# Kernel optimization log

Measured on AMD Instinct MI355X. Metric: run time of the kernel, lower is better.

## Reference

```python
import jax, jax.numpy as jnp
import numpy as np

B, K, T, V, R = 32, 3, 20, 10000, 36
E_DIM, VDIM, H1, H2, PH = 512, 2048, 1024, 1024, 256
START, EOS = 1, 2
NEG = -1e9


def lstm_cell(x, h, c, Wi, Wh, b):
    # torch LSTM gate order: i, f, g, o
    g = x @ Wi.T + h @ Wh.T + b
    i, f, gg, o = jnp.split(g, 4, axis=-1)
    c = jax.nn.sigmoid(f) * c + jax.nn.sigmoid(i) * jnp.tanh(gg)
    h = jax.nn.sigmoid(o) * jnp.tanh(c)
    return h, c


def _decode(features, E, Wi1, Wh1, b1, Wi2, Wh2, b2, Wva, bva, Wha, bha, wa, Wout, bout):
    featP = features @ Wva.T + bva                       # [B,R,PH] (step-invariant)
    vmean = jnp.broadcast_to(features.mean(1)[:, None, :], (B, K, VDIM))
    eos_row = jnp.full((V,), NEG, features.dtype).at[EOS].set(0.0)

    def step(carry, t):
        tokens, logp_traj, h1, c1, h2, c2, finished, trajs = carry
        emb = E[tokens]                                   # [B,K,E]
        x1 = jnp.concatenate([h2, vmean, emb], -1)        # [B,K,H2+VDIM+E]
        h1, c1 = lstm_cell(x1, h1, c1, Wi1, Wh1, b1)
        # additive attention over R regions
        hp = h1 @ Wha.T + bha                             # [B,K,PH]
        pre = jnp.tanh(featP[:, None] + hp[:, :, None])   # [B,K,R,PH]
        alpha = jax.nn.softmax(jnp.einsum('bkrp,p->bkr', pre, wa), -1)
        vhat = jnp.einsum('bkr,brd->bkd', alpha, features)
        x2 = jnp.concatenate([h1, vhat], -1)
        h2, c2 = lstm_cell(x2, h2, c2, Wi2, Wh2, b2)
        logp = jax.nn.log_softmax(h2 @ Wout.T + bout, -1)  # [B,K,V]
        # max_k_NoDuplicate: forbid repeating the previous token (only for t>0)
        dup = jax.nn.one_hot(tokens, V, dtype=logp.dtype) * jnp.where(t > 0, 1.0, 0.0)
        logp = logp - 1e4 * dup
        # EOS-terminated beams: only EOS with logprob 0, everything else -inf
        logp = jnp.where(finished[:, :, None], eos_row, logp)
        scores = logp_traj[:, :, None] + logp              # [B,K,V]
        # at t==0 all beams are identical -> keep only beam 0 as source
        beam_mask = ((jnp.arange(K) > 0)[None, :, None]) & (t == 0)
        scores = jnp.where(beam_mask, NEG, scores)
        vals, idx = jax.lax.top_k(scores.reshape(B, K * V), K)
        parent = idx // V
        tok = idx % V
        gather = lambda x: jnp.take_along_axis(x, parent[:, :, None], axis=1)
        h1, c1, h2, c2 = gather(h1), gather(c1), gather(h2), gather(c2)
        finished = jnp.take_along_axis(finished, parent, 1) | (tok == EOS)
        trajs = jnp.take_along_axis(trajs, parent[:, :, None], 1)
        trajs = jnp.where(jnp.arange(T)[None, None, :] == t, tok[:, :, None], trajs)
        return (tok, vals, h1, c1, h2, c2, finished, trajs), None

    z1 = jnp.zeros((B, K, H1), features.dtype)
    z2 = jnp.zeros((B, K, H2), features.dtype)
    init = (jnp.full((B, K), START, jnp.int32), jnp.zeros((B, K), features.dtype),
            z1, z1, z2, z2, jnp.zeros((B, K), bool), jnp.zeros((B, K, T), jnp.int32))
    carry, _ = jax.lax.scan(step, init, jnp.arange(T))
    _, logp_traj, _, _, _, _, _, trajs = carry
    return trajs.transpose(0, 2, 1), logp_traj  # [B,T,K] like torch.stack(Trajs,2), [B,K]


def setup_inputs():
    key = jax.random.key(0)
    ks = jax.random.split(key, 12)
    s = 0.05
    rn = lambda k, shp: jax.random.normal(k, shp, jnp.float32) * s
    return {
        'features': jax.random.normal(ks[0], (B, R, VDIM), jnp.float32),
        'E': rn(ks[1], (V, E_DIM)),
        'Wi1': rn(ks[2], (4 * H1, H2 + VDIM + E_DIM)),
        'Wh1': rn(ks[3], (4 * H1, H1)),
        'b1': jnp.zeros((4 * H1,), jnp.float32),
        'Wi2': rn(ks[4], (4 * H2, H1 + VDIM)),
        'Wh2': rn(ks[5], (4 * H2, H2)),
        'b2': jnp.zeros((4 * H2,), jnp.float32),
        'Wva': rn(ks[6], (PH, VDIM)),
        'bva': jnp.zeros((PH,), jnp.float32),
        'Wha': rn(ks[7], (PH, H1)),
        'bha': jnp.zeros((PH,), jnp.float32),
        'wa': rn(ks[8], (PH,)),
        'Wout': rn(ks[9], (V, H2)),
        'bout': jnp.zeros((V,), jnp.float32),
    }


def reference(features, E, Wi1, Wh1, b1, Wi2, Wh2, b2, Wva, bva, Wha, bha, wa, Wout, bout):
    return _decode(features, E, Wi1, Wh1, b1, Wi2, Wh2, b2, Wva, bva, Wha, bha, wa, Wout, bout)
```

## Files before the change

### kernel.cpp

```cpp
#include <hip/hip_runtime.h>
#include <math.h>

#define BB 32
#define KB 3
#define TT 20
#define VV 10000
#define RR 36
#define ED 512
#define VD 2048
#define HH 1024
#define PH_ 256
#define ROWS 96
#define EOS_TOK 2

struct Seg { const double* X; const float* W; int ldx; int ldw; int woff; int kbeg; };
struct GemmA { Seg seg[3]; int nseg; int Mtot; int N; int Ktot; };

#define GBN 64
#define GKC 32
#define PX 34
#define PW 36

__global__ __launch_bounds__(256) void gemm_f64(GemmA a, double* __restrict__ part) {
  __shared__ double Xs[96][PX];
  __shared__ float  Ws[GBN][PW];
  const int tid = threadIdx.x;
  const int n0 = blockIdx.x * GBN;
  const int s = blockIdx.y;
  const int m0 = blockIdx.z * 96;
  const int S = gridDim.y;
  const int ck = a.Ktot / S;
  const int ks = s * ck;
  const int nch = ck / GKC;
  const int tx = tid & 15, ty = tid >> 4;

  double acc[6][4];
#pragma unroll
  for (int r = 0; r < 6; ++r)
#pragma unroll
    for (int c = 0; c < 4; ++c) acc[r][c] = 0.0;

  double2 xst[6];
  float4 wst[2];

  auto issue = [&](int k0) {
    int si = 0;
    for (int i = 1; i < a.nseg; ++i) if (k0 >= a.seg[i].kbeg) si = i;
    Seg sg = a.seg[si];
    int kl = k0 - sg.kbeg;
#pragma unroll
    for (int j = 0; j < 6; ++j) {
      int i = tid + 256 * j;
      int m = i >> 4, q = (i & 15) << 1;
      int mg = m0 + m;
      double2 v; v.x = 0.0; v.y = 0.0;
      if (mg < a.Mtot) v = *(const double2*)&sg.X[(size_t)mg * sg.ldx + kl + q];
      xst[j] = v;
    }
#pragma unroll
    for (int j = 0; j < 2; ++j) {
      int i = tid + 256 * j;
      int n = i >> 3, q = (i & 7) << 2;
      int ng = n0 + n;
      float4 v = {0.f, 0.f, 0.f, 0.f};
      if (ng < a.N) v = *(const float4*)&sg.W[(size_t)ng * sg.ldw + sg.woff + kl + q];
      wst[j] = v;
    }
  };

  issue(ks);
  for (int ch = 0; ch < nch; ++ch) {
    __syncthreads();
#pragma unroll
    for (int j = 0; j < 6; ++j) {
      int i = tid + 256 * j;
      int m = i >> 4, q = (i & 15) << 1;
      *(double2*)&Xs[m][q] = xst[j];
    }
#pragma unroll
    for (int j = 0; j < 2; ++j) {
      int i = tid + 256 * j;
      int n = i >> 3, q = (i & 7) << 2;
      *(float4*)&Ws[n][q] = wst[j];
    }
    __syncthreads();
    if (ch + 1 < nch) issue(ks + (ch + 1) * GKC);
#pragma unroll
    for (int kq = 0; kq < GKC; kq += 4) {
      double wd[4][4];
#pragma unroll
      for (int c = 0; c < 4; ++c) {
        float4 w = *(const float4*)&Ws[tx + 16 * c][kq];
        wd[c][0] = (double)w.x; wd[c][1] = (double)w.y;
        wd[c][2] = (double)w.z; wd[c][3] = (double)w.w;
      }
#pragma unroll
      for (int r = 0; r < 6; ++r) {
        double2 x01 = *(const double2*)&Xs[ty * 6 + r][kq];
        double2 x23 = *(const double2*)&Xs[ty * 6 + r][kq + 2];
#pragma unroll
        for (int c = 0; c < 4; ++c) {
          acc[r][c] = fma(x01.x, wd[c][0], acc[r][c]);
          acc[r][c] = fma(x01.y, wd[c][1], acc[r][c]);
          acc[r][c] = fma(x23.x, wd[c][2], acc[r][c]);
          acc[r][c] = fma(x23.y, wd[c][3], acc[r][c]);
        }
      }
    }
  }
#pragma unroll
  for (int r = 0; r < 6; ++r) {
    int mg = m0 + ty * 6 + r;
    if (mg >= a.Mtot) continue;
    size_t base = ((size_t)s * a.Mtot + mg) * a.N;
#pragma unroll
    for (int c = 0; c < 4; ++c) {
      int ng = n0 + tx + 16 * c;
      if (ng < a.N) part[base + ng] = acc[r][c];
    }
  }
}

__global__ void convf_kernel(const float* __restrict__ s, double* __restrict__ d, int n) {
  int i = blockIdx.x * 256 + threadIdx.x;
  if (i < n) d[i] = (double)s[i];
}

__global__ void conv_kernel(const float* b1, const float* b2, const float* bva,
                            const float* bha, const float* wa, const float* bout,
                            double* b1d, double* b2d, double* bvad,
                            double* bhad, double* wad, double* boutd) {
  int i = blockIdx.x * 256 + threadIdx.x;
  if (i < 4 * HH) { b1d[i] = (double)b1[i]; b2d[i] = (double)b2[i]; }
  if (i < PH_) { bvad[i] = (double)bva[i]; bhad[i] = (double)bha[i]; wad[i] = (double)wa[i]; }
  if (i < VV) boutd[i] = (double)bout[i];
}

__global__ void init_kernel(double* h1s, double* c1s, double* h2s, double* c2s,
                            int* tok, double* lpt, int* fin, int* trj) {
  int idx = blockIdx.x * 256 + threadIdx.x;
  if (idx < ROWS * HH) { h1s[idx] = 0.0; c1s[idx] = 0.0; h2s[idx] = 0.0; c2s[idx] = 0.0; }
  if (idx < ROWS) { tok[idx] = 1; lpt[idx] = 0.0; fin[idx] = 0; }
  if (idx < ROWS * TT) trj[idx] = 0;
}

__global__ void vmean_kernel(const float* __restrict__ features, double* __restrict__ vme) {
  int idx = blockIdx.x * 256 + threadIdx.x;
  if (idx >= BB * VD) return;
  int b = idx / VD, d = idx - b * VD;
  double sum = 0.0;
  for (int r = 0; r < RR; ++r) sum += (double)features[((size_t)b * RR + r) * VD + d];
  vme[idx] = sum / (double)RR;
}

__global__ void reduce_bias_kernel(double* __restrict__ out, const double* __restrict__ parts,
                                   const double* __restrict__ bias, int rows, int cols, int S) {
  int idx = blockIdx.x * 256 + threadIdx.x;
  if (idx >= rows * cols) return;
  int c = idx % cols;
  double acc = bias[c];
  for (int s = 0; s < S; ++s) acc += parts[(size_t)s * rows * cols + idx];
  out[idx] = acc;
}

__global__ void embed_kernel(const int* __restrict__ tok, const float* __restrict__ E,
                             double* __restrict__ emb) {
  int idx = blockIdx.x * 256 + threadIdx.x;
  if (idx >= ROWS * ED) return;
  int row = idx >> 9, e2 = idx & (ED - 1);
  emb[idx] = (double)E[(size_t)tok[row] * ED + e2];
}

__global__ void lstm_kernel(const double* __restrict__ gP, int S,
                            const double* __restrict__ bias_col, const double* __restrict__ bias_row,
                            const double* __restrict__ c_in, double* __restrict__ h_out,
                            double* __restrict__ c_out) {
  int idx = blockIdx.x * 256 + threadIdx.x;
  if (idx >= ROWS * (HH / 2)) return;
  int row = idx >> 9, jj = (idx & 511) << 1;
  int b = row / KB;
  double2 g[4];
#pragma unroll
  for (int gi = 0; gi < 4; ++gi) {
    double2 acc;
    if (bias_col) acc = *(const double2*)&bias_col[gi * HH + jj];
    else          acc = *(const double2*)&bias_row[(size_t)b * 4 * HH + gi * HH + jj];
    for (int s = 0; s < S; ++s) {
      double2 p = *(const double2*)&gP[((size_t)s * ROWS + row) * (4 * HH) + gi * HH + jj];
      acc.x += p.x; acc.y += p.y;
    }
    g[gi] = acc;
  }
  double2 cp = *(const double2*)&c_in[((size_t)row << 10) + jj];
  double2 hv, cv;
  {
    double ig = 1.0 / (1.0 + exp(-g[0].x)), fg = 1.0 / (1.0 + exp(-g[1].x));
    double gg = tanh(g[2].x), og = 1.0 / (1.0 + exp(-g[3].x));
    cv.x = fg * cp.x + ig * gg; hv.x = og * tanh(cv.x);
  }
  {
    double ig = 1.0 / (1.0 + exp(-g[0].y)), fg = 1.0 / (1.0 + exp(-g[1].y));
    double gg = tanh(g[2].y), og = 1.0 / (1.0 + exp(-g[3].y));
    cv.y = fg * cp.y + ig * gg; hv.y = og * tanh(cv.y);
  }
  *(double2*)&h_out[((size_t)row << 10) + jj] = hv;
  *(double2*)&c_out[((size_t)row << 10) + jj] = cv;
}

__global__ __launch_bounds__(256) void attn_kernel(const double* __restrict__ hpP, int S,
    const double* __restrict__ bha, const double* __restrict__ featP,
    const float* __restrict__ features, const double* __restrict__ wa,
    double* __restrict__ vhat) {
  int row = blockIdx.x;
  int b = row / KB;
  int tid = threadIdx.x;
  __shared__ double hp[PH_];
  __shared__ double e[RR];
  {
    double v = bha[tid];
    for (int s = 0; s < S; ++s) v += hpP[((size_t)s * ROWS + row) * PH_ + tid];
    hp[tid] = v;
  }
  __syncthreads();
  int wv = tid >> 6, ln = tid & 63;
  for (int r = wv * 9; r < wv * 9 + 9; ++r) {
    double p = 0.0;
#pragma unroll
    for (int i = 0; i < 4; ++i) {
      int ph = ln * 4 + i;
      p += tanh(featP[((size_t)b * RR + r) * PH_ + ph] + hp[ph]) * wa[ph];
    }
#pragma unroll
    for (int o = 32; o; o >>= 1) p += __shfl_down(p, o);
    if (ln == 0) e[r] = p;
  }
  __syncthreads();
  if (tid == 0) {
    double m = e[0];
    for (int r = 1; r < RR; ++r) m = fmax(m, e[r]);
    double se = 0.0;
    for (int r = 0; r < RR; ++r) se += exp(e[r] - m);
    for (int r = 0; r < RR; ++r) e[r] = exp(e[r] - m) / se;
  }
  __syncthreads();
  for (int d = tid; d < VD; d += 256) {
    double acc2 = 0.0;
    for (int r = 0; r < RR; ++r) acc2 += e[r] * (double)features[((size_t)b * RR + r) * VD + d];
    vhat[(size_t)row * VD + d] = acc2;
  }
}

__device__ inline double wred_maxd(double v) {
#pragma unroll
  for (int o = 32; o; o >>= 1) v = fmax(v, __shfl_down(v, o));
  return v;
}
__device__ inline double wred_sumd(double v) {
#pragma unroll
  for (int o = 32; o; o >>= 1) v += __shfl_down(v, o);
  return v;
}

__device__ inline bool better(double va, int ia, double vb, int ib) {
  if (va != vb) return va > vb;
  return (unsigned)ia < (unsigned)ib;
}

__global__ __launch_bounds__(256) void lchunk_kernel(const double* __restrict__ lP, int S,
    const double* __restrict__ bout, const int* __restrict__ tok_old, int t,
    double* __restrict__ cm, double* __restrict__ cs,
    double* __restrict__ cv, int* __restrict__ ci) {
  const int CHV = VV / 8;
  int row = blockIdx.x, chk = blockIdx.y, tid = threadIdx.x;
  int v0 = chk * CHV;
  int tokp = tok_old[row];
  double r[5];
  double lmax = -1.0e300;
#pragma unroll
  for (int j = 0; j < 5; ++j) {
    int vv = tid + (j << 8);
    double acc = -1.0e300;
    if (vv < CHV) {
      int v = v0 + vv;
      acc = bout[v];
      for (int s = 0; s < S; ++s) acc += lP[((size_t)s * ROWS + row) * VV + v];
      lmax = fmax(lmax, acc);
    }
    r[j] = acc;
  }
  __shared__ double red[4];
  double m = wred_maxd(lmax);
  if ((tid & 63) == 0) red[tid >> 6] = m;
  __syncthreads();
  m = fmax(fmax(red[0], red[1]), fmax(red[2], red[3]));
  double se = 0.0;
#pragma unroll
  for (int j = 0; j < 5; ++j) {
    int vv = tid + (j << 8);
    if (vv < CHV) se += exp(r[j] - m);
  }
  se = wred_sumd(se);
  __syncthreads();
  if ((tid & 63) == 0) red[tid >> 6] = se;
  __syncthreads();
  se = red[0] + red[1] + red[2] + red[3];
  double lv[3] = {-INFINITY, -INFINITY, -INFINITY};
  int li[3] = {-1, -1, -1};
#pragma unroll
  for (int j = 0; j < 5; ++j) {
    int vv = tid + (j << 8);
    if (vv >= CHV) continue;
    int v = v0 + vv;
    double sc = r[j];
    if (t > 0 && v == tokp) sc -= 1e4;
    if (better(sc, v, lv[2], li[2])) {
      if (better(sc, v, lv[1], li[1])) {
        lv[2] = lv[1]; li[2] = li[1];
        if (better(sc, v, lv[0], li[0])) { lv[1] = lv[0]; li[1] = li[0]; lv[0] = sc; li[0] = v; }
        else { lv[1] = sc; li[1] = v; }
      } else { lv[2] = sc; li[2] = v; }
    }
  }
  __shared__ double sv[256 * 3];
  __shared__ int si[256 * 3];
  sv[tid * 3 + 0] = lv[0]; sv[tid * 3 + 1] = lv[1]; sv[tid * 3 + 2] = lv[2];
  si[tid * 3 + 0] = li[0]; si[tid * 3 + 1] = li[1]; si[tid * 3 + 2] = li[2];
  for (int off2 = 128; off2 >= 1; off2 >>= 1) {
    __syncthreads();
    if (tid < off2) {
      double av[3], bv2[3]; int ai3[3], bi3[3];
#pragma unroll
      for (int j = 0; j < 3; ++j) {
        av[j] = sv[tid * 3 + j]; ai3[j] = si[tid * 3 + j];
        bv2[j] = sv[(tid + off2) * 3 + j]; bi3[j] = si[(tid + off2) * 3 + j];
      }
      double mv[3]; int mi[3];
      int ai = 0, bi = 0;
#pragma unroll
      for (int o = 0; o < 3; ++o) {
        if (better(av[ai], ai3[ai], bv2[bi], bi3[bi])) { mv[o] = av[ai]; mi[o] = ai3[ai]; ++ai; }
        else { mv[o] = bv2[bi]; mi[o] = bi3[bi]; ++bi; }
      }
#pragma unroll
      for (int j = 0; j < 3; ++j) { sv[tid * 3 + j] = mv[j]; si[tid * 3 + j] = mi[j]; }
    }
  }
  __syncthreads();
  if (tid == 0) {
    int o = row * 8 + chk;
    cm[o] = m; cs[o] = se;
    cv[o * 3 + 0] = sv[0]; cv[o * 3 + 1] = sv[1]; cv[o * 3 + 2] = sv[2];
    ci[o * 3 + 0] = si[0]; ci[o * 3 + 1] = si[1]; ci[o * 3 + 2] = si[2];
  }
}

__global__ __launch_bounds__(64) void topk2_kernel(
    const double* __restrict__ cm, const double* __restrict__ cs,
    const double* __restrict__ cv, const int* __restrict__ ci,
    const double* __restrict__ lpt_old, const int* __restrict__ fin_old,
    const int* __restrict__ trj_old, int t,
    int* __restrict__ tok_new, double* __restrict__ lpt_new, int* __restrict__ fin_new,
    int* __restrict__ trj_new, int* __restrict__ parent) {
  int b = blockIdx.x, tid = threadIdx.x;
  __shared__ double candv[72];
  __shared__ int candi[72];
  __shared__ int cnt[3];
  __shared__ int fink[3];
  __shared__ int sp[3], stk[3];
  if (tid < KB) {
    int row = b * KB + tid;
    double lpt = lpt_old[row];
    int fin = fin_old[row];
    fink[tid] = fin;
    int base = tid * 24;
    if (t == 0 && tid > 0) {
      cnt[tid] = 0;
    } else if (fin) {
      candv[base] = lpt;
      candi[base] = tid * VV + EOS_TOK;
      cnt[tid] = 1;
    } else {
      double M = -1.0e300;
      for (int c = 0; c < 8; ++c) M = fmax(M, cm[row * 8 + c]);
      double SE = 0.0;
      for (int c = 0; c < 8; ++c) SE += cs[row * 8 + c] * exp(cm[row * 8 + c] - M);
      double l = log(SE);
      int n = 0;
      for (int c = 0; c < 8; ++c) {
#pragma unroll
        for (int s3 = 0; s3 < 3; ++s3) {
          double val = cv[(row * 8 + c) * 3 + s3];
          int idx = ci[(row * 8 + c) * 3 + s3];
          candv[base + n] = lpt + ((val - M) - l);
          candi[base + n] = tid * VV + idx;
          ++n;
        }
      }
      cnt[tid] = n;
    }
  }
  __syncthreads();
  if (tid == 0) {
    double bv[3] = {-INFINITY, -INFINITY, -INFINITY};
    int bi2[3] = {-1, -1, -1};
    for (int k = 0; k < KB; ++k) {
      for (int j = 0; j < cnt[k]; ++j) {
        double sc = candv[k * 24 + j];
        int idx = candi[k * 24 + j];
        if (better(sc, idx, bv[2], bi2[2])) {
          if (better(sc, idx, bv[1], bi2[1])) {
            bv[2] = bv[1]; bi2[2] = bi2[1];
            if (better(sc, idx, bv[0], bi2[0])) { bv[1] = bv[0]; bi2[1] = bi2[0]; bv[0] = sc; bi2[0] = idx; }
            else { bv[1] = sc; bi2[1] = idx; }
          } else { bv[2] = sc; bi2[2] = idx; }
        }
      }
    }
#pragma unroll
    for (int o = 0; o < 3; ++o) {
      int idx = bi2[o];
      int p = idx / VV, tk = idx - p * VV;
      sp[o] = p; stk[o] = tk;
      parent[b * KB + o] = p;
      tok_new[b * KB + o] = tk;
      lpt_new[b * KB + o] = bv[o];
      fin_new[b * KB + o] = fink[p] | (tk == EOS_TOK);
    }
  }
  __syncthreads();
  if (tid < KB * TT) {
    int kk = tid / TT, tt = tid - kk * TT;
    trj_new[(b * KB + kk) * TT + tt] = (tt == t) ? stk[kk] : trj_old[(b * KB + sp[kk]) * TT + tt];
  }
}

__global__ void gather_kernel(const int* __restrict__ parent,
    const double* __restrict__ h1p, const double* __restrict__ c1p,
    const double* __restrict__ h2p, const double* __restrict__ c2p,
    double* __restrict__ h1s, double* __restrict__ c1s,
    double* __restrict__ h2s, double* __restrict__ c2s) {
  int idx = blockIdx.x * 256 + threadIdx.x;
  if (idx >= ROWS * (HH / 2)) return;
  int row = idx >> 9, jj = (idx & 511) << 1;
  int b = row / KB;
  int p = parent[row];
  size_t src = ((size_t)(b * KB + p) << 10) + jj;
  size_t dst = ((size_t)row << 10) + jj;
  *(double2*)&h1s[dst] = *(const double2*)&h1p[src];
  *(double2*)&c1s[dst] = *(const double2*)&c1p[src];
  *(double2*)&h2s[dst] = *(const double2*)&h2p[src];
  *(double2*)&c2s[dst] = *(const double2*)&c2p[src];
}

__global__ void out_kernel(const int* __restrict__ trj, const double* __restrict__ lpt,
                           float* __restrict__ out) {
  int idx = blockIdx.x * 256 + threadIdx.x;
  if (idx < BB * TT * KB) {
    int k = idx % KB;
    int rest = idx / KB;
    int t = rest % TT;
    int b = rest / TT;
    out[idx] = (float)trj[((size_t)(b * KB + k)) * TT + t];
  }
  if (idx < ROWS) out[BB * TT * KB + idx] = (float)lpt[idx];
}

extern "C" void kernel_launch(void* const* d_in, const int* in_sizes, int n_in,
                              void* d_out, int out_size, void* d_ws, size_t ws_size,
                              hipStream_t stream) {
  const float* features = (const float*)d_in[0];
  const float* E = (const float*)d_in[1];
  const float* Wi1 = (const float*)d_in[2];
  const float* Wh1 = (const float*)d_in[3];
  const float* b1 = (const float*)d_in[4];
  const float* Wi2 = (const float*)d_in[5];
  const float* Wh2 = (const float*)d_in[6];
  const float* b2 = (const float*)d_in[7];
  const float* Wva = (const float*)d_in[8];
  const float* bva = (const float*)d_in[9];
  const float* Wha = (const float*)d_in[10];
  const float* bha = (const float*)d_in[11];
  const float* wa = (const float*)d_in[12];
  const float* Wout = (const float*)d_in[13];
  const float* bout = (const float*)d_in[14];
  float* out = (float*)d_out;

  const int SF = 4, SV = 8, S1 = 8, SH = 32, S2 = 8, SL = 4;

  double* base = (double*)d_ws;
  size_t off = 0;
  auto A = [&](size_t n) { double* p = base + off; off += n; return p; };
  double* featP = A((size_t)BB * RR * PH_);
  double* vme = A((size_t)BB * VD);
  double* gv1 = A((size_t)BB * 4 * HH);
  double* emb96 = A((size_t)ROWS * ED);
  double* vhat = A((size_t)ROWS * VD);
  double* h1s = A((size_t)ROWS * HH);
  double* c1s = A((size_t)ROWS * HH);
  double* h2s = A((size_t)ROWS * HH);
  double* c2s = A((size_t)ROWS * HH);
  double* h1p = A((size_t)ROWS * HH);
  double* c1p = A((size_t)ROWS * HH);
  double* h2p = A((size_t)ROWS * HH);
  double* c2p = A((size_t)ROWS * HH);
  double* b1d = A(4 * HH);
  double* b2d = A(4 * HH);
  double* bvad = A(PH_);
  double* bhad = A(PH_);
  double* wad = A(PH_);
  double* boutd = A(VV);
  double* cmS = A((size_t)ROWS * 8);
  double* csS = A((size_t)ROWS * 8);
  double* cvS = A((size_t)ROWS * 8 * 3);
  size_t arena_sz = (size_t)S1 * ROWS * 4 * HH;
  { size_t t2 = (size_t)S2 * ROWS * 4 * HH; if (t2 > arena_sz) arena_sz = t2; }
  { size_t tl = (size_t)SL * ROWS * VV;     if (tl > arena_sz) arena_sz = tl; }
  { size_t tv = (size_t)SV * BB * 4 * HH;   if (tv > arena_sz) arena_sz = tv; }
  { size_t tp = (size_t)BB * RR * VD + (size_t)SF * BB * RR * PH_;
    if (tp > arena_sz) arena_sz = tp; }
  double* arena = A(arena_sz);
  double* featF = arena;
  double* pF2 = arena + (size_t)BB * RR * VD;
  double* pV = arena;
  double* pG = arena;
  double* pL = arena;
  double* pH = A((size_t)SH * ROWS * PH_);
  double* lptA = A(ROWS);
  double* lptB = A(ROWS);
  int* ip = (int*)(base + off);
  int* tokA = ip; ip += ROWS;
  int* tokB = ip; ip += ROWS;
  int* finA = ip; ip += ROWS;
  int* finB = ip; ip += ROWS;
  int* par = ip; ip += ROWS;
  int* ciS = ip; ip += ROWS * 8 * 3;
  int* trjA = ip; ip += ROWS * TT;
  int* trjB = ip; ip += ROWS * TT;

  init_kernel<<<(ROWS * HH + 255) / 256, 256, 0, stream>>>(h1s, c1s, h2s, c2s, tokA, lptA, finA, trjA);
  conv_kernel<<<(VV + 255) / 256, 256, 0, stream>>>(b1, b2, bva, bha, wa, bout,
                                                    b1d, b2d, bvad, bhad, wad, boutd);
  vmean_kernel<<<(BB * VD + 255) / 256, 256, 0, stream>>>(features, vme);
  convf_kernel<<<(BB * RR * VD + 255) / 256, 256, 0, stream>>>(features, featF, BB * RR * VD);
  {
    GemmA a{};
    a.seg[0] = Seg{featF, Wva, VD, VD, 0, 0};
    a.nseg = 1; a.Mtot = BB * RR; a.N = PH_; a.Ktot = VD;
    dim3 g((PH_ + GBN - 1) / GBN, SF, (BB * RR + 95) / 96);
    gemm_f64<<<g, 256, 0, stream>>>(a, pF2);
    reduce_bias_kernel<<<(BB * RR * PH_ + 255) / 256, 256, 0, stream>>>(featP, pF2, bvad, BB * RR, PH_, SF);
  }
  {
    GemmA a{};
    a.seg[0] = Seg{vme, Wi1, VD, 3584, 1024, 0};
    a.nseg = 1; a.Mtot = BB; a.N = 4 * HH; a.Ktot = VD;
    dim3 g((4 * HH + GBN - 1) / GBN, SV, 1);
    gemm_f64<<<g, 256, 0, stream>>>(a, pV);
    reduce_bias_kernel<<<(BB * 4 * HH + 255) / 256, 256, 0, stream>>>(gv1, pV, b1d, BB, 4 * HH, SV);
  }

  int *tokC = tokA, *tokN = tokB, *finC = finA, *finN = finB, *trjC = trjA, *trjN = trjB;
  double *lptC = lptA, *lptN = lptB;
  for (int t = 0; t < TT; ++t) {
    embed_kernel<<<(ROWS * ED + 255) / 256, 256, 0, stream>>>(tokC, E, emb96);
    {
      GemmA a{};
      a.seg[0] = Seg{h2s, Wi1, HH, 3584, 0, 0};
      a.seg[1] = Seg{emb96, Wi1, ED, 3584, 3072, 1024};
      a.seg[2] = Seg{h1s, Wh1, HH, HH, 0, 1536};
      a.nseg = 3; a.Mtot = ROWS; a.N = 4 * HH; a.Ktot = 2560;
      dim3 g((4 * HH + GBN - 1) / GBN, S1, 1);
      gemm_f64<<<g, 256, 0, stream>>>(a, pG);
    }
    lstm_kernel<<<(ROWS * (HH / 2) + 255) / 256, 256, 0, stream>>>(pG, S1, nullptr, gv1, c1s, h1p, c1p);
    {
      GemmA a{};
      a.seg[0] = Seg{h1p, Wha, HH, HH, 0, 0};
      a.nseg = 1; a.Mtot = ROWS; a.N = PH_; a.Ktot = HH;
      dim3 g((PH_ + GBN - 1) / GBN, SH, 1);
      gemm_f64<<<g, 256, 0, stream>>>(a, pH);
    }
    attn_kernel<<<ROWS, 256, 0, stream>>>(pH, SH, bhad, featP, features, wad, vhat);
    {
      GemmA a{};
      a.seg[0] = Seg{h1p, Wi2, HH, 3072, 0, 0};
      a.seg[1] = Seg{vhat, Wi2, VD, 3072, 1024, 1024};
      a.seg[2] = Seg{h2s, Wh2, HH, HH, 0, 3072};
      a.nseg = 3; a.Mtot = ROWS; a.N = 4 * HH; a.Ktot = 4096;
      dim3 g((4 * HH + GBN - 1) / GBN, S2, 1);
      gemm_f64<<<g, 256, 0, stream>>>(a, pG);
    }
    lstm_kernel<<<(ROWS * (HH / 2) + 255) / 256, 256, 0, stream>>>(pG, S2, b2d, nullptr, c2s, h2p, c2p);
    {
      GemmA a{};
      a.seg[0] = Seg{h2p, Wout, HH, HH, 0, 0};
      a.nseg = 1; a.Mtot = ROWS; a.N = VV; a.Ktot = HH;
      dim3 g((VV + GBN - 1) / GBN, SL, 1);
      gemm_f64<<<g, 256, 0, stream>>>(a, pL);
    }
    lchunk_kernel<<<dim3(ROWS, 8), 256, 0, stream>>>(pL, SL, boutd, tokC, t, cmS, csS, cvS, ciS);
    topk2_kernel<<<BB, 64, 0, stream>>>(cmS, csS, cvS, ciS, lptC, finC, trjC, t,
                                        tokN, lptN, finN, trjN, par);
    gather_kernel<<<(ROWS * (HH / 2) + 255) / 256, 256, 0, stream>>>(par, h1p, c1p, h2p, c2p,
                                                                     h1s, c1s, h2s, c2s);
    { int* tmp; double* tf;
      tmp = tokC; tokC = tokN; tokN = tmp;
      tmp = finC; finC = finN; finN = tmp;
      tmp = trjC; trjC = trjN; trjN = tmp;
      tf = lptC; lptC = lptN; lptN = tf; }
  }
  out_kernel<<<(BB * TT * KB + 255) / 256, 256, 0, stream>>>(trjC, lptC, out);
}
```

Measured before the change: 6.355 ms.

## Halve GEMM N-tile and convert weight tile to double in shared memory

Reduces the FP64 GEMM block's N tile from 64 to 32 columns, giving each thread 6x2 accumulators instead of 6x4. Weights are converted from float to double once when written to shared memory instead of on every read in the inner loop. This doubles the number of blocks to improve occupancy and latency hiding, and cuts per-thread conversion work. In exchange it lowers register-level reuse of the X tile and raises the total global X loads across blocks.

```diff
diff --git a/kernel.cpp b/kernel.cpp
--- a/kernel.cpp
+++ b/kernel.cpp
@@ -16,14 +16,14 @@
 struct Seg { const double* X; const float* W; int ldx; int ldw; int woff; int kbeg; };
 struct GemmA { Seg seg[3]; int nseg; int Mtot; int N; int Ktot; };
 
-#define GBN 64
+#define GBN 32
 #define GKC 32
 #define PX 34
-#define PW 36
+#define PWD 34
 
 __global__ __launch_bounds__(256) void gemm_f64(GemmA a, double* __restrict__ part) {
   __shared__ double Xs[96][PX];
-  __shared__ float  Ws[GBN][PW];
+  __shared__ double Ws[GBN][PWD];
   const int tid = threadIdx.x;
   const int n0 = blockIdx.x * GBN;
   const int s = blockIdx.y;
@@ -34,14 +34,12 @@
   const int nch = ck / GKC;
   const int tx = tid & 15, ty = tid >> 4;
 
-  double acc[6][4];
-#pragma unroll
-  for (int r = 0; r < 6; ++r)
-#pragma unroll
-    for (int c = 0; c < 4; ++c) acc[r][c] = 0.0;
+  double acc[6][2];
+#pragma unroll
+  for (int r = 0; r < 6; ++r) { acc[r][0] = 0.0; acc[r][1] = 0.0; }
 
   double2 xst[6];
-  float4 wst[2];
+  float4 wst;
 
   auto issue = [&](int k0) {
     int si = 0;
@@ -57,14 +55,12 @@
       if (mg < a.Mtot) v = *(const double2*)&sg.X[(size_t)mg * sg.ldx + kl + q];
       xst[j] = v;
     }
-#pragma unroll
-    for (int j = 0; j < 2; ++j) {
-      int i = tid + 256 * j;
-      int n = i >> 3, q = (i & 7) << 2;
+    {
+      int n = tid >> 3, q = (tid & 7) << 2;
       int ng = n0 + n;
       float4 v = {0.f, 0.f, 0.f, 0.f};
       if (ng < a.N) v = *(const float4*)&sg.W[(size_t)ng * sg.ldw + sg.woff + kl + q];
-      wst[j] = v;
+      wst = v;
     }
   };
 
@@ -77,34 +73,34 @@
       int m = i >> 4, q = (i & 15) << 1;
       *(double2*)&Xs[m][q] = xst[j];
     }
-#pragma unroll
-    for (int j = 0; j < 2; ++j) {
-      int i = tid + 256 * j;
-      int n = i >> 3, q = (i & 7) << 2;
-      *(float4*)&Ws[n][q] = wst[j];
+    {
+      int n = tid >> 3, q = (tid & 7) << 2;
+      double2 w01, w23;
+      w01.x = (double)wst.x; w01.y = (double)wst.y;
+      w23.x = (double)wst.z; w23.y = (double)wst.w;
+      *(double2*)&Ws[n][q] = w01;
+      *(double2*)&Ws[n][q + 2] = w23;
     }
     __syncthreads();
     if (ch + 1 < nch) issue(ks + (ch + 1) * GKC);
 #pragma unroll
     for (int kq = 0; kq < GKC; kq += 4) {
-      double wd[4][4];
-#pragma unroll
-      for (int c = 0; c < 4; ++c) {
-        float4 w = *(const float4*)&Ws[tx + 16 * c][kq];
-        wd[c][0] = (double)w.x; wd[c][1] = (double)w.y;
-        wd[c][2] = (double)w.z; wd[c][3] = (double)w.w;
-      }
+      double2 w0a = *(const double2*)&Ws[tx][kq];
+      double2 w0b = *(const double2*)&Ws[tx][kq + 2];
+      double2 w1a = *(const double2*)&Ws[tx + 16][kq];
+      double2 w1b = *(const double2*)&Ws[tx + 16][kq + 2];
 #pragma unroll
       for (int r = 0; r < 6; ++r) {
         double2 x01 = *(const double2*)&Xs[ty * 6 + r][kq];
         double2 x23 = *(const double2*)&Xs[ty * 6 + r][kq + 2];
-#pragma unroll
-        for (int c = 0; c < 4; ++c) {
-          acc[r][c] = fma(x01.x, wd[c][0], acc[r][c]);
-          acc[r][c] = fma(x01.y, wd[c][1], acc[r][c]);
-          acc[r][c] = fma(x23.x, wd[c][2], acc[r][c]);
-          acc[r][c] = fma(x23.y, wd[c][3], acc[r][c]);
-        }
+        acc[r][0] = fma(x01.x, w0a.x, acc[r][0]);
+        acc[r][0] = fma(x01.y, w0a.y, acc[r][0]);
+        acc[r][0] = fma(x23.x, w0b.x, acc[r][0]);
+        acc[r][0] = fma(x23.y, w0b.y, acc[r][0]);
+        acc[r][1] = fma(x01.x, w1a.x, acc[r][1]);
+        acc[r][1] = fma(x01.y, w1a.y, acc[r][1]);
+        acc[r][1] = fma(x23.x, w1b.x, acc[r][1]);
+        acc[r][1] = fma(x23.y, w1b.y, acc[r][1]);
       }
     }
   }
@@ -114,7 +110,7 @@
     if (mg >= a.Mtot) continue;
     size_t base = ((size_t)s * a.Mtot + mg) * a.N;
 #pragma unroll
-    for (int c = 0; c < 4; ++c) {
+    for (int c = 0; c < 2; ++c) {
       int ng = n0 + tx + 16 * c;
       if (ng < a.N) part[base + ng] = acc[r][c];
     }
```

Result: slower. 6.847 ms (+7.7%).

## Use FP64 MFMA instructions in the split-K GEMM inner loop

Applied to the files above, without the earlier changes.

Replaces the scalar double-precision FMA micro-tile in gemm_f64 with __builtin_amdgcn_mfma_f64_16x16x4f64 calls. Each wave now owns a 16-column slice and six 16-row tiles. The output register layout is found at runtime by a small probe kernel that writes row and column maps, which the epilogue reads. This targets the FP64 FMA throughput limit of the GEMMs. The costs are scalar LDS loads with possible bank conflicts and a dependence on the probe mapping being correct.

```diff
diff --git a/kernel.cpp b/kernel.cpp
--- a/kernel.cpp
+++ b/kernel.cpp
@@ -13,6 +13,8 @@
 #define ROWS 96
 #define EOS_TOK 2
 
+typedef double f64x4 __attribute__((ext_vector_type(4)));
+
 struct Seg { const double* X; const float* W; int ldx; int ldw; int woff; int kbeg; };
 struct GemmA { Seg seg[3]; int nseg; int Mtot; int N; int Ktot; };
 
@@ -21,7 +23,22 @@
 #define PX 34
 #define PW 36
 
-__global__ __launch_bounds__(256) void gemm_f64(GemmA a, double* __restrict__ part) {
+__global__ void mfma_probe(int* __restrict__ rowmap, int* __restrict__ colmap) {
+  int lane = threadIdx.x & 63;
+  f64x4 z = {0.0, 0.0, 0.0, 0.0};
+  double a1 = (double)(lane & 15), b1 = 1.0;
+  f64x4 d1 = __builtin_amdgcn_mfma_f64_16x16x4f64(a1, b1, z, 0, 0, 0);
+  double a2 = 1.0, b2 = (double)(lane & 15);
+  f64x4 d2 = __builtin_amdgcn_mfma_f64_16x16x4f64(a2, b2, z, 0, 0, 0);
+#pragma unroll
+  for (int r = 0; r < 4; ++r) {
+    rowmap[lane * 4 + r] = (int)(d1[r] * 0.25 + 0.5);
+    colmap[lane * 4 + r] = (int)(d2[r] * 0.25 + 0.5);
+  }
+}
+
+__global__ __launch_bounds__(256) void gemm_f64(GemmA a, double* __restrict__ part,
+    const int* __restrict__ rowmap, const int* __restrict__ colmap) {
   __shared__ double Xs[96][PX];
   __shared__ float  Ws[GBN][PW];
   const int tid = threadIdx.x;
@@ -32,13 +49,12 @@
   const int ck = a.Ktot / S;
   const int ks = s * ck;
   const int nch = ck / GKC;
-  const int tx = tid & 15, ty = tid >> 4;
-
-  double acc[6][4];
-#pragma unroll
-  for (int r = 0; r < 6; ++r)
-#pragma unroll
-    for (int c = 0; c < 4; ++c) acc[r][c] = 0.0;
+  const int wave = tid >> 6, lane = tid & 63;
+  const int lrow = lane & 15, lk = lane >> 4;
+
+  f64x4 acc[6];
+#pragma unroll
+  for (int r = 0; r < 6; ++r) acc[r] = (f64x4){0.0, 0.0, 0.0, 0.0};
 
   double2 xst[6];
   float4 wst[2];
@@ -87,36 +103,25 @@
     if (ch + 1 < nch) issue(ks + (ch + 1) * GKC);
 #pragma unroll
     for (int kq = 0; kq < GKC; kq += 4) {
-      double wd[4][4];
-#pragma unroll
-      for (int c = 0; c < 4; ++c) {
-        float4 w = *(const float4*)&Ws[tx + 16 * c][kq];
-        wd[c][0] = (double)w.x; wd[c][1] = (double)w.y;
-        wd[c][2] = (double)w.z; wd[c][3] = (double)w.w;
+      double b = (double)Ws[16 * wave + lrow][kq + lk];
+#pragma unroll
+      for (int r = 0; r < 6; ++r) {
+        double av = Xs[16 * r + lrow][kq + lk];
+        acc[r] = __builtin_amdgcn_mfma_f64_16x16x4f64(av, b, acc[r], 0, 0, 0);
       }
-#pragma unroll
-      for (int r = 0; r < 6; ++r) {
-        double2 x01 = *(const double2*)&Xs[ty * 6 + r][kq];
-        double2 x23 = *(const double2*)&Xs[ty * 6 + r][kq + 2];
-#pragma unroll
-        for (int c = 0; c < 4; ++c) {
-          acc[r][c] = fma(x01.x, wd[c][0], acc[r][c]);
-          acc[r][c] = fma(x01.y, wd[c][1], acc[r][c]);
-          acc[r][c] = fma(x23.x, wd[c][2], acc[r][c]);
-          acc[r][c] = fma(x23.y, wd[c][3], acc[r][c]);
-        }
-      }
-    }
-  }
+    }
+  }
+  int rmap[4], cmap[4];
+#pragma unroll
+  for (int i = 0; i < 4; ++i) { rmap[i] = rowmap[lane * 4 + i]; cmap[i] = colmap[lane * 4 + i]; }
 #pragma unroll
   for (int r = 0; r < 6; ++r) {
-    int mg = m0 + ty * 6 + r;
-    if (mg >= a.Mtot) continue;
-    size_t base = ((size_t)s * a.Mtot + mg) * a.N;
-#pragma unroll
-    for (int c = 0; c < 4; ++c) {
-      int ng = n0 + tx + 16 * c;
-      if (ng < a.N) part[base + ng] = acc[r][c];
+#pragma unroll
+    for (int i = 0; i < 4; ++i) {
+      int mg = m0 + 16 * r + rmap[i];
+      int col = n0 + 16 * wave + cmap[i];
+      if (mg < a.Mtot && col < a.N)
+        part[((size_t)s * a.Mtot + mg) * a.N + col] = acc[r][i];
     }
   }
 }
@@ -536,7 +541,10 @@
   int* ciS = ip; ip += ROWS * 8 * 3;
   int* trjA = ip; ip += ROWS * TT;
   int* trjB = ip; ip += ROWS * TT;
-
+  int* rowmap = ip; ip += 256;
+  int* colmap = ip; ip += 256;
+
+  mfma_probe<<<1, 64, 0, stream>>>(rowmap, colmap);
   init_kernel<<<(ROWS * HH + 255) / 256, 256, 0, stream>>>(h1s, c1s, h2s, c2s, tokA, lptA, finA, trjA);
   conv_kernel<<<(VV + 255) / 256, 256, 0, stream>>>(b1, b2, bva, bha, wa, bout,
                                                     b1d, b2d, bvad, bhad, wad, boutd);
@@ -547,7 +555,7 @@
     a.seg[0] = Seg{featF, Wva, VD, VD, 0, 0};
     a.nseg = 1; a.Mtot = BB * RR; a.N = PH_; a.Ktot = VD;
     dim3 g((PH_ + GBN - 1) / GBN, SF, (BB * RR + 95) / 96);
-    gemm_f64<<<g, 256, 0, stream>>>(a, pF2);
+    gemm_f64<<<g, 256, 0, stream>>>(a, pF2, rowmap, colmap);
     reduce_bias_kernel<<<(BB * RR * PH_ + 255) / 256, 256, 0, stream>>>(featP, pF2, bvad, BB * RR, PH_, SF);
   }
   {
@@ -555,7 +563,7 @@
     a.seg[0] = Seg{vme, Wi1, VD, 3584, 1024, 0};
     a.nseg = 1; a.Mtot = BB; a.N = 4 * HH; a.Ktot = VD;
     dim3 g((4 * HH + GBN - 1) / GBN, SV, 1);
-    gemm_f64<<<g, 256, 0, stream>>>(a, pV);
+    gemm_f64<<<g, 256, 0, stream>>>(a, pV, rowmap, colmap);
     reduce_bias_kernel<<<(BB * 4 * HH + 255) / 256, 256, 0, stream>>>(gv1, pV, b1d, BB, 4 * HH, SV);
   }
 
@@ -570,7 +578,7 @@
       a.seg[2] = Seg{h1s, Wh1, HH, HH, 0, 1536};
       a.nseg = 3; a.Mtot = ROWS; a.N = 4 * HH; a.Ktot = 2560;
       dim3 g((4 * HH + GBN - 1) / GBN, S1, 1);
-      gemm_f64<<<g, 256, 0, stream>>>(a, pG);
+      gemm_f64<<<g, 256, 0, stream>>>(a, pG, rowmap, colmap);
     }
     lstm_kernel<<<(ROWS * (HH / 2) + 255) / 256, 256, 0, stream>>>(pG, S1, nullptr, gv1, c1s, h1p, c1p);
     {
@@ -578,7 +586,7 @@
       a.seg[0] = Seg{h1p, Wha, HH, HH, 0, 0};
       a.nseg = 1; a.Mtot = ROWS; a.N = PH_; a.Ktot = HH;
       dim3 g((PH_ + GBN - 1) / GBN, SH, 1);
-      gemm_f64<<<g, 256, 0, stream>>>(a, pH);
+      gemm_f64<<<g, 256, 0, stream>>>(a, pH, rowmap, colmap);
     }
     attn_kernel<<<ROWS, 256, 0, stream>>>(pH, SH, bhad, featP, features, wad, vhat);
     {
@@ -588,7 +596,7 @@
       a.seg[2] = Seg{h2s, Wh2, HH, HH, 0, 3072};
       a.nseg = 3; a.Mtot = ROWS; a.N = 4 * HH; a.Ktot = 4096;
       dim3 g((4 * HH + GBN - 1) / GBN, S2, 1);
-      gemm_f64<<<g, 256, 0, stream>>>(a, pG);
+      gemm_f64<<<g, 256, 0, stream>>>(a, pG, rowmap, colmap);
     }
     lstm_kernel<<<(ROWS * (HH / 2) + 255) / 256, 256, 0, stream>>>(pG, S2, b2d, nullptr, c2s, h2p, c2p);
     {
@@ -596,7 +604,7 @@
       a.seg[0] = Seg{h2p, Wout, HH, HH, 0, 0};
       a.nseg = 1; a.Mtot = ROWS; a.N = VV; a.Ktot = HH;
       dim3 g((VV + GBN - 1) / GBN, SL, 1);
-      gemm_f64<<<g, 256, 0, stream>>>(a, pL);
+      gemm_f64<<<g, 256, 0, stream>>>(a, pL, rowmap, colmap);
     }
     lchunk_kernel<<<dim3(ROWS, 8), 256, 0, stream>>>(pL, SL, boutd, tokC, t, cmS, csS, cvS, ciS);
     topk2_kernel<<<BB, 64, 0, stream>>>(cmS, csS, cvS, ciS, lptC, finC, trjC, t,
```

New measurement: 5.303 ms. -16.5%, faster.
